# Optimization experiments

Hardware: AMD Instinct MI355X
Metric: run time of the kernel (lower is better)

Reference implementation:

```python
import jax, jax.numpy as jnp
import numpy as np

NUM_FIELDS = 24
OP = "circular_convolution"  # or "circular_correlation"

# upper-triangular (i<j) field pair indices, matching torch.triu_indices(F, F, offset=1)
_I, _J = np.triu_indices(NUM_FIELDS, k=1)
_IDX0 = jnp.asarray(_I, dtype=jnp.int32)  # [P], P = F*(F-1)/2 = 276
_IDX1 = jnp.asarray(_J, dtype=jnp.int32)


def setup_inputs() -> dict:
    key = jax.random.key(0)
    inputs = jax.random.normal(key, (2048, NUM_FIELDS, 64), dtype=jnp.float32)
    return {"inputs": inputs}


def reference(inputs):
    # inputs: [B, F, D]; gather pairwise field embeddings -> [B, P, D]
    emb0 = inputs[:, _IDX0, :]
    emb1 = inputs[:, _IDX1, :]
    fft0 = jnp.fft.fft(emb0)  # complex64, FFT along D
    fft1 = jnp.fft.fft(emb1)
    if OP == "circular_correlation":
        fft0 = jnp.conj(fft0)
    # circular convolution/correlation via frequency-domain product; real part of ifft
    return jnp.real(jnp.fft.ifft(fft0 * fft1))  # [B, P, D]
```

## Files before the change

kernel.cpp:

```cpp
#include <hip/hip_runtime.h>
#include <stdint.h>


typedef __bf16 bf16x8 __attribute__((ext_vector_type(8)));
typedef float  f32x4  __attribute__((ext_vector_type(4)));

#define NF       24
#define DIM      64
#define NPAIR    276
#define RSTRIDE  264
#define XB_OFF   (NF * RSTRIDE)
#define XB_STRIDE 72
#define LDS_BYTES (XB_OFF + 32 * XB_STRIDE * 2)

__global__ __launch_bounds__(256)
void holo_fm_kernel(const float* __restrict__ in, float* __restrict__ out)
{
    __shared__ __align__(16) unsigned char lds[LDS_BYTES];
    __bf16* xb = (__bf16*)(lds + XB_OFF);

    const int tid = threadIdx.x;
    const int b   = blockIdx.x;
    const float* xin = in + (size_t)b * (NF * DIM);

    for (int e = tid; e < (32 - NF) * XB_STRIDE; e += 256)
        xb[NF * XB_STRIDE + e] = (__bf16)0.0f;

    for (int e = tid; e < NF * DIM; e += 256) {
        int i = e >> 6, m = e & 63;
        __bf16 v = (__bf16)xin[e];
        xb[i * XB_STRIDE + m] = v;
        __bf16* rj = (__bf16*)(lds + i * RSTRIDE);
        int u0 = (64 - m) & 63;
        rj[u0]      = v;
        rj[u0 + 64] = v;
    }
    __syncthreads();

    const int lane = tid & 63;
    const int wave = tid >> 6;
    const int ln   = lane & 15;
    const int q    = lane >> 4;

    bf16x8 afrag[2][2];
    #pragma unroll
    for (int it = 0; it < 2; ++it)
        #pragma unroll
        for (int ks = 0; ks < 2; ++ks)
            afrag[it][ks] = *(const bf16x8*)(xb + (it * 16 + ln) * XB_STRIDE + ks * 32 + q * 8);

    for (int j = wave + 1; j < NF; j += 4) {
        const uint64_t* rj = (const uint64_t*)(lds + j * RSTRIDE);
        #pragma unroll
        for (int nt = 0; nt < 4; ++nt) {
            const int n = nt * 16 + ln;
            bf16x8 bfr[2];
            #pragma unroll
            for (int ks = 0; ks < 2; ++ks) {
                int ob = 2 * (64 + 32 * ks + 8 * q - n);
                int dw = ob >> 3;
                int sh = (ob & 7) * 8;
                uint64_t w0 = rj[dw], w1 = rj[dw + 1], w2 = rj[dw + 2];
                uint64_t lo = (w0 >> sh) | ((w1 << 1) << (63 - sh));
                uint64_t hi = (w1 >> sh) | ((w2 << 1) << (63 - sh));
                union { uint64_t u[2]; bf16x8 v; } cv;
                cv.u[0] = lo; cv.u[1] = hi;
                bfr[ks] = cv.v;
            }

            float* ob0 = out + ((size_t)b * NPAIR) * DIM + n;

            f32x4 c0 = {0.f, 0.f, 0.f, 0.f};
            c0 = __builtin_amdgcn_mfma_f32_16x16x32_bf16(afrag[0][0], bfr[0], c0, 0, 0, 0);
            c0 = __builtin_amdgcn_mfma_f32_16x16x32_bf16(afrag[0][1], bfr[1], c0, 0, 0, 0);
            #pragma unroll
            for (int r = 0; r < 4; ++r) {
                int i = 4 * q + r;
                if (i < j) {
                    int pidx = 23 * i - (i * (i - 1)) / 2 + (j - i - 1);
                    ob0[(size_t)pidx * DIM] = c0[r];
                }
            }

            if (j > 16) {
                f32x4 c1 = {0.f, 0.f, 0.f, 0.f};
                c1 = __builtin_amdgcn_mfma_f32_16x16x32_bf16(afrag[1][0], bfr[0], c1, 0, 0, 0);
                c1 = __builtin_amdgcn_mfma_f32_16x16x32_bf16(afrag[1][1], bfr[1], c1, 0, 0, 0);
                #pragma unroll
                for (int r = 0; r < 4; ++r) {
                    int i = 16 + 4 * q + r;
                    if (i < j) {
                        int pidx = 23 * i - (i * (i - 1)) / 2 + (j - i - 1);
                        ob0[(size_t)pidx * DIM] = c1[r];
                    }
                }
            }
        }
    }
}

extern "C" void kernel_launch(void* const* d_in, const int* in_sizes, int n_in,
                              void* d_out, int out_size, void* d_ws, size_t ws_size,
                              hipStream_t stream)
{
    const float* in  = (const float*)d_in[0];
    float*       out = (float*)d_out;
    const int batches = in_sizes[0] / (NF * DIM);
    holo_fm_kernel<<<dim3(batches), dim3(256), 0, stream>>>(in, out);
}
```

Before: 161.6 us.

## Transpose MFMA roles so each lane stores contiguous float4 output rows

Swaps the operand roles so the circulant window of field i becomes the A operand and the raw embeddings of field j become B. Each lane's 4 accumulator values are now 4 consecutive output elements, so results are written with 16-byte vector stores instead of scattered scalar stores. The loop also now runs over i rather than j. That lets the six shifted windows be built once per i and reused across all output tiles, cutting the redundant bit-shift window construction. The price is more live registers for the window array and an uneven split of i rows across the four waves.

Result: no change. 159.1 us (-1.5%).

```diff
diff --git a/kernel.cpp b/kernel.cpp
--- a/kernel.cpp
+++ b/kernel.cpp
@@ -27,13 +27,13 @@
         xb[NF * XB_STRIDE + e] = (__bf16)0.0f;
 
     for (int e = tid; e < NF * DIM; e += 256) {
-        int i = e >> 6, m = e & 63;
+        int f = e >> 6, m = e & 63;
         __bf16 v = (__bf16)xin[e];
-        xb[i * XB_STRIDE + m] = v;
-        __bf16* rj = (__bf16*)(lds + i * RSTRIDE);
+        xb[f * XB_STRIDE + m] = v;
+        __bf16* rr = (__bf16*)(lds + f * RSTRIDE);
         int u0 = (64 - m) & 63;
-        rj[u0]      = v;
-        rj[u0 + 64] = v;
+        rr[u0]      = v;
+        rr[u0 + 64] = v;
     }
     __syncthreads();
 
@@ -42,58 +42,45 @@
     const int ln   = lane & 15;
     const int q    = lane >> 4;
 
-    bf16x8 afrag[2][2];
+    bf16x8 bfrag[2][2];
     #pragma unroll
-    for (int it = 0; it < 2; ++it)
+    for (int jt = 0; jt < 2; ++jt)
         #pragma unroll
         for (int ks = 0; ks < 2; ++ks)
-            afrag[it][ks] = *(const bf16x8*)(xb + (it * 16 + ln) * XB_STRIDE + ks * 32 + q * 8);
+            bfrag[jt][ks] = *(const bf16x8*)(xb + (jt * 16 + ln) * XB_STRIDE + ks * 32 + q * 8);
 
-    for (int j = wave + 1; j < NF; j += 4) {
-        const uint64_t* rj = (const uint64_t*)(lds + j * RSTRIDE);
+    float* gbase = out + (size_t)b * NPAIR * DIM;
+
+    for (int i = wave; i < NF - 1; i += 4) {
+        const uint64_t* ri = (const uint64_t*)(lds + i * RSTRIDE);
+        const int p0 = 23 * i - (i * (i - 1)) / 2;
+
+        bf16x8 awin[6];
         #pragma unroll
-        for (int nt = 0; nt < 4; ++nt) {
-            const int n = nt * 16 + ln;
-            bf16x8 bfr[2];
+        for (int w = 0; w < 6; ++w) {
+            int ob = 2 * (16 * (w + 1) + 8 * q - ln);
+            int dw = ob >> 3;
+            int sh = (ob & 7) * 8;
+            uint64_t w0 = ri[dw], w1 = ri[dw + 1], w2 = ri[dw + 2];
+            uint64_t lo = (w0 >> sh) | ((w1 << 1) << (63 - sh));
+            uint64_t hi = (w1 >> sh) | ((w2 << 1) << (63 - sh));
+            union { uint64_t u[2]; bf16x8 v; } cv;
+            cv.u[0] = lo; cv.u[1] = hi;
+            awin[w] = cv.v;
+        }
+
+        const int jtlo = (i < 15) ? 0 : 1;
+        for (int jt = jtlo; jt < 2; ++jt) {
+            const int j = 16 * jt + ln;
+            const bool valid = (j > i) & (j < NF);
+            float* orow = gbase + ((size_t)(p0 + j - i - 1)) * DIM + 4 * q;
             #pragma unroll
-            for (int ks = 0; ks < 2; ++ks) {
-                int ob = 2 * (64 + 32 * ks + 8 * q - n);
-                int dw = ob >> 3;
-                int sh = (ob & 7) * 8;
-                uint64_t w0 = rj[dw], w1 = rj[dw + 1], w2 = rj[dw + 2];
-                uint64_t lo = (w0 >> sh) | ((w1 << 1) << (63 - sh));
-                uint64_t hi = (w1 >> sh) | ((w2 << 1) << (63 - sh));
-                union { uint64_t u[2]; bf16x8 v; } cv;
-                cv.u[0] = lo; cv.u[1] = hi;
-                bfr[ks] = cv.v;
-            }
-
-            float* ob0 = out + ((size_t)b * NPAIR) * DIM + n;
-
-            f32x4 c0 = {0.f, 0.f, 0.f, 0.f};
-            c0 = __builtin_amdgcn_mfma_f32_16x16x32_bf16(afrag[0][0], bfr[0], c0, 0, 0, 0);
-            c0 = __builtin_amdgcn_mfma_f32_16x16x32_bf16(afrag[0][1], bfr[1], c0, 0, 0, 0);
-            #pragma unroll
-            for (int r = 0; r < 4; ++r) {
-                int i = 4 * q + r;
-                if (i < j) {
-                    int pidx = 23 * i - (i * (i - 1)) / 2 + (j - i - 1);
-                    ob0[(size_t)pidx * DIM] = c0[r];
-                }
-            }
-
-            if (j > 16) {
-                f32x4 c1 = {0.f, 0.f, 0.f, 0.f};
-                c1 = __builtin_amdgcn_mfma_f32_16x16x32_bf16(afrag[1][0], bfr[0], c1, 0, 0, 0);
-                c1 = __builtin_amdgcn_mfma_f32_16x16x32_bf16(afrag[1][1], bfr[1], c1, 0, 0, 0);
-                #pragma unroll
-                for (int r = 0; r < 4; ++r) {
-                    int i = 16 + 4 * q + r;
-                    if (i < j) {
-                        int pidx = 23 * i - (i * (i - 1)) / 2 + (j - i - 1);
-                        ob0[(size_t)pidx * DIM] = c1[r];
-                    }
-                }
+            for (int mt = 0; mt < 4; ++mt) {
+                f32x4 c = {0.f, 0.f, 0.f, 0.f};
+                c = __builtin_amdgcn_mfma_f32_16x16x32_bf16(awin[3 - mt], bfrag[jt][0], c, 0, 0, 0);
+                c = __builtin_amdgcn_mfma_f32_16x16x32_bf16(awin[5 - mt], bfrag[jt][1], c, 0, 0, 0);
+                if (valid)
+                    *(f32x4*)(orow + 16 * mt) = c;
             }
         }
     }
```
